# Kernel tuning notes

Measured on AMD Instinct MI355X. Metric: run time of the kernel, lower is better.

Reference implementation:

```python
import jax, jax.numpy as jnp
import numpy as np

B, C, H, W = 32, 512, 32, 32
N_WORDS, WORD_DIM = 77, 256
HW2 = H * W


def setup_inputs() -> dict:
    key = jax.random.key(0)
    k1, k2, k3 = jax.random.split(key, 3)
    feat = jax.random.normal(k1, (B, C, H, W), dtype=jnp.float32)
    word_emb = jax.random.normal(k2, (B, N_WORDS, WORD_DIM), dtype=jnp.float32)
    # nn.Linear(word_dim, img_hw*img_hw): weight (out,in), bias (out,)
    W_fc = jax.random.normal(k3, (HW2, WORD_DIM), dtype=jnp.float32) * (1.0 / np.sqrt(WORD_DIM))
    b_fc = jnp.zeros((HW2,), dtype=jnp.float32)
    return {"feat": feat, "word_emb": word_emb, "W_fc": W_fc, "b_fc": b_fc}


def reference(feat, word_emb, W_fc, b_fc):
    b, c, h, w = feat.shape
    f = feat.reshape(b, c, h * w)                                   # (b, c, hw2)
    we = jnp.einsum('bnd,kd->bnk', word_emb, W_fc) + b_fc           # (b, n, hw2)
    we = jnp.swapaxes(we, 1, 2)                                     # (b, hw2, n)
    scores = jnp.einsum('bck,bkn->bcn', f, we)                      # (b, c, n)
    att = jax.nn.softmax(scores, axis=-1)                           # (b, c, n)
    att_feat = jnp.einsum('bcn,bkn->bck', att, we)                  # (b, c, hw2)
    return att_feat.reshape(b, c, h, w)
```

## Files before the change

kernel.cpp:

```cpp
#include <hip/hip_runtime.h>

#define B_    32
#define C_    512
#define HW2_  1024
#define NW    77
#define NP    80
#define NPT   96
#define WD    256

typedef unsigned int   uint32;
typedef unsigned short u16;
typedef __attribute__((ext_vector_type(8))) short bf16x8;
typedef __attribute__((ext_vector_type(4))) float f32x4;

#define MFMA(a, b, c) __builtin_amdgcn_mfma_f32_16x16x32_bf16(a, b, c, 0, 0, 0)

#define WE_ELN   ((size_t)B_ * 16 * NP * 8)
#define WET_ELN  ((size_t)B_ * HW2_ * 12)

__device__ __forceinline__ void split1(float x, u16 &h, u16 &l) {
    uint32 u = __float_as_uint(x);
    h = (u16)(u >> 16);
    float r = x - __uint_as_float(u & 0xffff0000u);
    uint32 v = __float_as_uint(r);
    l = (u16)((v + 0x7fffu + ((v >> 16) & 1u)) >> 16);
}

__device__ __forceinline__ void split8(float4 a, float4 b, bf16x8 &h, bf16x8 &l) {
    float v[8] = {a.x, a.y, a.z, a.w, b.x, b.y, b.z, b.w};
    #pragma unroll
    for (int i = 0; i < 8; ++i) {
        u16 hh, ll; split1(v[i], hh, ll);
        h[i] = (short)hh; l[i] = (short)ll;
    }
}

__global__ __launch_bounds__(256, 2) void we_gemm(
    const float* __restrict__ word_emb, const float* __restrict__ W_fc,
    const float* __restrict__ b_fc,
    bf16x8* __restrict__ we_hi, bf16x8* __restrict__ we_lo,
    bf16x8* __restrict__ weT_hi, bf16x8* __restrict__ weT_lo)
{
    __shared__ __align__(16) uint32 HL[NP][68];

    const int id = blockIdx.x;
    const int b  = (id & 7) + 8 * (id >> 7);
    const int q  = (id >> 3) & 15;
    const int kb = q * 64;
    const int t  = threadIdx.x;
    const int w  = t >> 6, lane = t & 63, lr = lane & 15, lg = lane >> 4;
    const int kout = kb + 16 * w + lr;

    const float* wrow = W_fc + kout * WD;
    float4 wx[8], wy[8];
    #pragma unroll
    for (int ks = 0; ks < 8; ++ks) {
        const int dk = ks * 32 + 8 * lg;
        wx[ks] = *(const float4*)(wrow + dk);
        wy[ks] = *(const float4*)(wrow + dk + 4);
    }
    __builtin_amdgcn_sched_barrier(0);

    bf16x8 bh[8], bl[8];
    #pragma unroll
    for (int ks = 0; ks < 8; ++ks) split8(wx[ks], wy[ks], bh[ks], bl[ks]);

    f32x4 acc[5];
    #pragma unroll
    for (int m = 0; m < 5; ++m) acc[m] = (f32x4)0.0f;

    const float* emb = word_emb + b * NW * WD;

    #pragma unroll
    for (int ks = 0; ks < 8; ++ks) {
        const int dk = ks * 32 + 8 * lg;
        bf16x8 ah[5], al[5];
        #pragma unroll
        for (int m = 0; m < 5; ++m) {
            const int n = 16 * m + lr;
            float4 x = make_float4(0.f, 0.f, 0.f, 0.f), y = x;
            if (n < NW) {
                const float* p = emb + n * WD + dk;
                x = *(const float4*)p; y = *(const float4*)(p + 4);
            }
            split8(x, y, ah[m], al[m]);
        }
        #pragma unroll
        for (int m = 0; m < 5; ++m) {
            acc[m] = MFMA(ah[m], bh[ks], acc[m]);
            acc[m] = MFMA(ah[m], bl[ks], acc[m]);
            acc[m] = MFMA(al[m], bh[ks], acc[m]);
            acc[m] = MFMA(al[m], bl[ks], acc[m]);
        }
    }

    const float bias = b_fc[kout];
    #pragma unroll
    for (int m = 0; m < 5; ++m)
        #pragma unroll
        for (int r = 0; r < 4; ++r) {
            u16 hh, ll; split1(acc[m][r] + bias, hh, ll);
            HL[16 * m + 4 * lg + r][16 * w + lr] = ((uint32)hh << 16) | ll;
        }
    __syncthreads();

    #pragma unroll
    for (int u0 = 0; u0 < 640; u0 += 256) {
        const int u = u0 + t;
        if (u < 640) {
            const int n = u >> 3, c8 = (u & 7) * 8;
            uint4 p0 = *(const uint4*)&HL[n][c8];
            uint4 p1 = *(const uint4*)&HL[n][c8 + 4];
            const uint32 pw[8] = {p0.x, p0.y, p0.z, p0.w, p1.x, p1.y, p1.z, p1.w};
            bf16x8 hv, lv;
            #pragma unroll
            for (int i = 0; i < 8; ++i) {
                hv[i] = (short)(pw[i] >> 16);
                lv[i] = (short)(pw[i] & 0xffffu);
            }
            const int o = ((b * 16 + q) * NP + n) * 8 + (u & 7);
            we_hi[o] = hv; we_lo[o] = lv;
        }
    }
    #pragma unroll
    for (int v0 = 0; v0 < 1536; v0 += 256) {
        const int v = v0 + t;
        const int sel = v >= 768;
        const int r2  = sel ? v - 768 : v;
        const int row = r2 / 12, g = r2 % 12;
        bf16x8 val;
        #pragma unroll
        for (int i = 0; i < 8; ++i) {
            const int n = g * 8 + i;
            const uint32 p = (n < NP) ? HL[n][row] : 0u;
            val[i] = (short)(sel ? (p & 0xffffu) : (p >> 16));
        }
        (sel ? weT_lo : weT_hi)[(b * HW2_ + kb + row) * 12 + g] = val;
    }
}

__global__ __launch_bounds__(256, 2) void attn_mfma(
    const float* __restrict__ feat,
    const bf16x8* __restrict__ we_hi, const bf16x8* __restrict__ we_lo,
    const bf16x8* __restrict__ weT_hi, const bf16x8* __restrict__ weT_lo,
    float* __restrict__ out)
{
    __shared__ __align__(16) float S[4][16][84];
    __shared__ __align__(16) u16   Ph[32][NPT];
    __shared__ __align__(16) u16   Pl[32][NPT];

    const int id  = blockIdx.x;
    const int b   = (id & 7) + 8 * (id >> 7);
    const int c0  = ((id >> 3) & 15) * 32;

    const int t    = threadIdx.x;
    const int h    = t >> 6;
    const int lane = t & 63, lr = lane & 15, lg = lane >> 4;

    const float* frow0 = feat + (size_t)(b * C_ + c0 + lr) * HW2_;
    const float* frow1 = frow0 + 16 * HW2_;

    float4 f0x[8], f0y[8], f1x[8], f1y[8];
    #pragma unroll
    for (int ks = 0; ks < 8; ++ks) {
        const int kk = h * 256 + ks * 32 + 8 * lg;
        f0x[ks] = *(const float4*)(frow0 + kk);
        f0y[ks] = *(const float4*)(frow0 + kk + 4);
        f1x[ks] = *(const float4*)(frow1 + kk);
        f1y[ks] = *(const float4*)(frow1 + kk + 4);
    }
    __builtin_amdgcn_sched_barrier(0);

    f32x4 acc[2][5];
    #pragma unroll
    for (int s = 0; s < 2; ++s)
        #pragma unroll
        for (int m = 0; m < 5; ++m) acc[s][m] = (f32x4)0.0f;

    #pragma unroll
    for (int ks = 0; ks < 8; ++ks) {
        bf16x8 fh0, fl0, fh1, fl1;
        split8(f0x[ks], f0y[ks], fh0, fl0);
        split8(f1x[ks], f1y[ks], fh1, fl1);
        const int qb  = (b * 16 + h * 4 + (ks >> 1)) * NP;
        const int sub = (ks & 1) * 4 + lg;
        #pragma unroll
        for (int m = 0; m < 5; ++m) {
            const int o = (qb + 16 * m + lr) * 8 + sub;
            const bf16x8 ah = we_hi[o];
            const bf16x8 al = we_lo[o];
            acc[0][m] = MFMA(ah, fh0, acc[0][m]);
            acc[0][m] = MFMA(ah, fl0, acc[0][m]);
            acc[0][m] = MFMA(al, fh0, acc[0][m]);
            acc[1][m] = MFMA(ah, fh1, acc[1][m]);
            acc[1][m] = MFMA(ah, fl1, acc[1][m]);
            acc[1][m] = MFMA(al, fh1, acc[1][m]);
        }
    }

    #pragma unroll
    for (int s = 0; s < 2; ++s) {
        #pragma unroll
        for (int m = 0; m < 5; ++m)
            #pragma unroll
            for (int r = 0; r < 4; ++r)
                S[h][lr][16 * m + 4 * lg + r] = acc[s][m][r];
        __syncthreads();
        {
            const int srow = 4 * h + (lane >> 4), scol = lane & 15;
            float v5[6];
            float mx = -3.0e38f;
            #pragma unroll
            for (int j = 0; j < 6; ++j) {
                const int n = scol + 16 * j;
                float sv = 0.f;
                if (j < 5) {
                    sv = S[0][srow][n] + S[1][srow][n] + S[2][srow][n] + S[3][srow][n];
                    if (n < NW) mx = fmaxf(mx, sv);
                }
                v5[j] = sv;
            }
            mx = fmaxf(mx, __shfl_xor(mx, 1));
            mx = fmaxf(mx, __shfl_xor(mx, 2));
            mx = fmaxf(mx, __shfl_xor(mx, 4));
            mx = fmaxf(mx, __shfl_xor(mx, 8));
            float sum = 0.f;
            #pragma unroll
            for (int j = 0; j < 6; ++j) {
                const int n = scol + 16 * j;
                const float e = (n < NW) ? __expf(v5[j] - mx) : 0.f;
                v5[j] = e; sum += e;
            }
            sum += __shfl_xor(sum, 1);
            sum += __shfl_xor(sum, 2);
            sum += __shfl_xor(sum, 4);
            sum += __shfl_xor(sum, 8);
            const float inv = 1.0f / sum;
            #pragma unroll
            for (int j = 0; j < 6; ++j) {
                const int n = scol + 16 * j;
                u16 ph, pl; split1(v5[j] * inv, ph, pl);
                Ph[16 * s + srow][n] = ph; Pl[16 * s + srow][n] = pl;
            }
        }
        __syncthreads();
    }

    bf16x8 pbh[2][3], pbl[2][3];
    #pragma unroll
    for (int s = 0; s < 2; ++s)
        #pragma unroll
        for (int ksn = 0; ksn < 3; ++ksn) {
            pbh[s][ksn] = *(const bf16x8*)&Ph[16 * s + lr][32 * ksn + 8 * lg];
            pbl[s][ksn] = *(const bf16x8*)&Pl[16 * s + lr][32 * ksn + 8 * lg];
        }
    const bf16x8* th = weT_hi + (size_t)b * HW2_ * 12;
    const bf16x8* tl = weT_lo + (size_t)b * HW2_ * 12;
    float* orow0 = out + (size_t)(b * C_ + c0 + lr) * HW2_;
    float* orow1 = orow0 + 16 * HW2_;

    #pragma unroll
    for (int tt = 0; tt < 16; ++tt) {
        const int row = h * 256 + tt * 16 + lr;
        bf16x8 wa[3], wb[3];
        #pragma unroll
        for (int ksn = 0; ksn < 3; ++ksn) {
            wa[ksn] = th[row * 12 + 4 * ksn + lg];
            wb[ksn] = tl[row * 12 + 4 * ksn + lg];
        }
        f32x4 o0 = (f32x4)0.0f, o1 = (f32x4)0.0f;
        #pragma unroll
        for (int ksn = 0; ksn < 3; ++ksn) {
            o0 = MFMA(wa[ksn], pbh[0][ksn], o0);
            o0 = MFMA(wa[ksn], pbl[0][ksn], o0);
            o0 = MFMA(wb[ksn], pbh[0][ksn], o0);
            o1 = MFMA(wa[ksn], pbh[1][ksn], o1);
            o1 = MFMA(wa[ksn], pbl[1][ksn], o1);
            o1 = MFMA(wb[ksn], pbh[1][ksn], o1);
        }
        const int col = h * 256 + tt * 16 + 4 * lg;
        *(float4*)(orow0 + col) = make_float4(o0[0], o0[1], o0[2], o0[3]);
        *(float4*)(orow1 + col) = make_float4(o1[0], o1[1], o1[2], o1[3]);
    }
}

extern "C" void kernel_launch(void* const* d_in, const int* in_sizes, int n_in,
                              void* d_out, int out_size, void* d_ws, size_t ws_size,
                              hipStream_t stream) {
    (void)in_sizes; (void)n_in; (void)out_size; (void)ws_size;
    const float* feat     = (const float*)d_in[0];
    const float* word_emb = (const float*)d_in[1];
    const float* W_fc     = (const float*)d_in[2];
    const float* b_fc     = (const float*)d_in[3];

    bf16x8* we_hi  = (bf16x8*)d_ws;
    bf16x8* we_lo  = we_hi  + WE_ELN;
    bf16x8* weT_hi = we_lo  + WE_ELN;
    bf16x8* weT_lo = weT_hi + WET_ELN;

    we_gemm<<<512, 256, 0, stream>>>(word_emb, W_fc, b_fc, we_hi, we_lo, weT_hi, weT_lo);
    attn_mfma<<<512, 256, 0, stream>>>(feat, we_hi, we_lo, weT_hi, weT_lo, (float*)d_out);
}
```

Before: 184.3 us.

## Software-pipeline global loads with register ring buffers and scheduling barriers

Restructures the inner loops of both kernels into prefetch pipelines. The word-embedding GEMM double-buffers embedding loads. The attention kernel now streams feature loads three stages deep instead of preloading all of them, and double-buffers the we tiles. The output stage triple-buffers the weT loads. Scheduling barriers pin the load and MFMA order so that memory latency overlaps with the matrix ops. The kernels hold fewer feature registers up front but keep more loads in flight, and the barriers can block useful reordering by the compiler.

```diff
diff --git a/kernel.cpp b/kernel.cpp
--- a/kernel.cpp
+++ b/kernel.cpp
@@ -14,6 +14,7 @@
 typedef __attribute__((ext_vector_type(4))) float f32x4;
 
 #define MFMA(a, b, c) __builtin_amdgcn_mfma_f32_16x16x32_bf16(a, b, c, 0, 0, 0)
+#define SWALL() __builtin_amdgcn_sched_barrier(0)
 
 #define WE_ELN   ((size_t)B_ * 16 * NP * 8)
 #define WET_ELN  ((size_t)B_ * HW2_ * 12)
@@ -59,8 +60,7 @@
         wx[ks] = *(const float4*)(wrow + dk);
         wy[ks] = *(const float4*)(wrow + dk + 4);
     }
-    __builtin_amdgcn_sched_barrier(0);
-
+    SWALL();
     bf16x8 bh[8], bl[8];
     #pragma unroll
     for (int ks = 0; ks < 8; ++ks) split8(wx[ks], wy[ks], bh[ks], bl[ks]);
@@ -71,20 +71,32 @@
 
     const float* emb = word_emb + b * NW * WD;
 
+    float4 ex[2][5], ey[2][5];
+#define WG_E(sl, ksv) do {                                          \
+        const int dk_ = (ksv) * 32 + 8 * lg;                        \
+        _Pragma("unroll")                                           \
+        for (int m_ = 0; m_ < 5; ++m_) {                            \
+            const int n_ = 16 * m_ + lr;                            \
+            if (n_ < NW) {                                          \
+                const float* p_ = emb + n_ * WD + dk_;              \
+                ex[sl][m_] = *(const float4*)p_;                    \
+                ey[sl][m_] = *(const float4*)(p_ + 4);              \
+            } else {                                                \
+                ex[sl][m_] = make_float4(0.f, 0.f, 0.f, 0.f);       \
+                ey[sl][m_] = make_float4(0.f, 0.f, 0.f, 0.f);       \
+            }                                                       \
+        } } while (0)
+
+    WG_E(0, 0);
+    SWALL();
     #pragma unroll
     for (int ks = 0; ks < 8; ++ks) {
-        const int dk = ks * 32 + 8 * lg;
+        const int cur = ks & 1;
+        if (ks < 7) WG_E(cur ^ 1, ks + 1);
+        SWALL();
         bf16x8 ah[5], al[5];
         #pragma unroll
-        for (int m = 0; m < 5; ++m) {
-            const int n = 16 * m + lr;
-            float4 x = make_float4(0.f, 0.f, 0.f, 0.f), y = x;
-            if (n < NW) {
-                const float* p = emb + n * WD + dk;
-                x = *(const float4*)p; y = *(const float4*)(p + 4);
-            }
-            split8(x, y, ah[m], al[m]);
-        }
+        for (int m = 0; m < 5; ++m) split8(ex[cur][m], ey[cur][m], ah[m], al[m]);
         #pragma unroll
         for (int m = 0; m < 5; ++m) {
             acc[m] = MFMA(ah[m], bh[ks], acc[m]);
@@ -92,7 +104,9 @@
             acc[m] = MFMA(al[m], bh[ks], acc[m]);
             acc[m] = MFMA(al[m], bl[ks], acc[m]);
         }
-    }
+        SWALL();
+    }
+#undef WG_E
 
     const float bias = b_fc[kout];
     #pragma unroll
@@ -160,43 +174,55 @@
     const float* frow0 = feat + (size_t)(b * C_ + c0 + lr) * HW2_;
     const float* frow1 = frow0 + 16 * HW2_;
 
-    float4 f0x[8], f0y[8], f1x[8], f1y[8];
+    float4 fx0[3], fy0[3], fx1[3], fy1[3];
+    bf16x8 wph[2][5], wpl[2][5];
+
+#define P1_FEAT(sl, ksv) do {                                       \
+        const int kk_ = h * 256 + (ksv) * 32 + 8 * lg;              \
+        fx0[sl] = *(const float4*)(frow0 + kk_);                    \
+        fy0[sl] = *(const float4*)(frow0 + kk_ + 4);                \
+        fx1[sl] = *(const float4*)(frow1 + kk_);                    \
+        fy1[sl] = *(const float4*)(frow1 + kk_ + 4); } while (0)
+#define P1_WE(sl, ksv) do {                                         \
+        const int qb_  = (b * 16 + h * 4 + ((ksv) >> 1)) * NP;      \
+        const int sub_ = ((ksv) & 1) * 4 + lg;                      \
+        _Pragma("unroll")                                           \
+        for (int m_ = 0; m_ < 5; ++m_) {                            \
+            const int o_ = (qb_ + 16 * m_ + lr) * 8 + sub_;         \
+            wph[sl][m_] = we_hi[o_];                                \
+            wpl[sl][m_] = we_lo[o_];                                \
+        } } while (0)
+
+    f32x4 acc[2][5];
+    #pragma unroll
+    for (int s = 0; s < 2; ++s)
+        #pragma unroll
+        for (int m = 0; m < 5; ++m) acc[s][m] = (f32x4)0.0f;
+
+    P1_FEAT(0, 0); P1_FEAT(1, 1); P1_WE(0, 0);
+    SWALL();
     #pragma unroll
     for (int ks = 0; ks < 8; ++ks) {
-        const int kk = h * 256 + ks * 32 + 8 * lg;
-        f0x[ks] = *(const float4*)(frow0 + kk);
-        f0y[ks] = *(const float4*)(frow0 + kk + 4);
-        f1x[ks] = *(const float4*)(frow1 + kk);
-        f1y[ks] = *(const float4*)(frow1 + kk + 4);
-    }
-    __builtin_amdgcn_sched_barrier(0);
-
-    f32x4 acc[2][5];
-    #pragma unroll
-    for (int s = 0; s < 2; ++s)
-        #pragma unroll
-        for (int m = 0; m < 5; ++m) acc[s][m] = (f32x4)0.0f;
-
-    #pragma unroll
-    for (int ks = 0; ks < 8; ++ks) {
+        const int fc = ks % 3, wc = ks & 1;
+        if (ks < 6) P1_FEAT((ks + 2) % 3, ks + 2);
+        if (ks < 7) P1_WE(wc ^ 1, ks + 1);
+        SWALL();
         bf16x8 fh0, fl0, fh1, fl1;
-        split8(f0x[ks], f0y[ks], fh0, fl0);
-        split8(f1x[ks], f1y[ks], fh1, fl1);
-        const int qb  = (b * 16 + h * 4 + (ks >> 1)) * NP;
-        const int sub = (ks & 1) * 4 + lg;
+        split8(fx0[fc], fy0[fc], fh0, fl0);
+        split8(fx1[fc], fy1[fc], fh1, fl1);
         #pragma unroll
         for (int m = 0; m < 5; ++m) {
-            const int o = (qb + 16 * m + lr) * 8 + sub;
-            const bf16x8 ah = we_hi[o];
-            const bf16x8 al = we_lo[o];
-            acc[0][m] = MFMA(ah, fh0, acc[0][m]);
-            acc[0][m] = MFMA(ah, fl0, acc[0][m]);
-            acc[0][m] = MFMA(al, fh0, acc[0][m]);
-            acc[1][m] = MFMA(ah, fh1, acc[1][m]);
-            acc[1][m] = MFMA(ah, fl1, acc[1][m]);
-            acc[1][m] = MFMA(al, fh1, acc[1][m]);
-        }
-    }
+            acc[0][m] = MFMA(wph[wc][m], fh0, acc[0][m]);
+            acc[0][m] = MFMA(wph[wc][m], fl0, acc[0][m]);
+            acc[0][m] = MFMA(wpl[wc][m], fh0, acc[0][m]);
+            acc[1][m] = MFMA(wph[wc][m], fh1, acc[1][m]);
+            acc[1][m] = MFMA(wph[wc][m], fl1, acc[1][m]);
+            acc[1][m] = MFMA(wpl[wc][m], fh1, acc[1][m]);
+        }
+        SWALL();
+    }
+#undef P1_FEAT
+#undef P1_WE
 
     #pragma unroll
     for (int s = 0; s < 2; ++s) {
@@ -259,29 +285,38 @@
     float* orow0 = out + (size_t)(b * C_ + c0 + lr) * HW2_;
     float* orow1 = orow0 + 16 * HW2_;
 
+    bf16x8 wa[3][3], wb[3][3];
+#define P3_LOAD(sl, ttv) do {                                       \
+        const int row_ = h * 256 + (ttv) * 16 + lr;                 \
+        _Pragma("unroll")                                           \
+        for (int k_ = 0; k_ < 3; ++k_) {                            \
+            wa[sl][k_] = th[row_ * 12 + 4 * k_ + lg];               \
+            wb[sl][k_] = tl[row_ * 12 + 4 * k_ + lg];               \
+        } } while (0)
+
+    P3_LOAD(0, 0); P3_LOAD(1, 1);
+    SWALL();
     #pragma unroll
     for (int tt = 0; tt < 16; ++tt) {
-        const int row = h * 256 + tt * 16 + lr;
-        bf16x8 wa[3], wb[3];
+        const int cur = tt % 3;
+        if (tt < 14) P3_LOAD((tt + 2) % 3, tt + 2);
+        SWALL();
+        f32x4 o0 = (f32x4)0.0f, o1 = (f32x4)0.0f;
         #pragma unroll
         for (int ksn = 0; ksn < 3; ++ksn) {
-            wa[ksn] = th[row * 12 + 4 * ksn + lg];
-            wb[ksn] = tl[row * 12 + 4 * ksn + lg];
-        }
-        f32x4 o0 = (f32x4)0.0f, o1 = (f32x4)0.0f;
-        #pragma unroll
-        for (int ksn = 0; ksn < 3; ++ksn) {
-            o0 = MFMA(wa[ksn], pbh[0][ksn], o0);
-            o0 = MFMA(wa[ksn], pbl[0][ksn], o0);
-            o0 = MFMA(wb[ksn], pbh[0][ksn], o0);
-            o1 = MFMA(wa[ksn], pbh[1][ksn], o1);
-            o1 = MFMA(wa[ksn], pbl[1][ksn], o1);
-            o1 = MFMA(wb[ksn], pbh[1][ksn], o1);
+            o0 = MFMA(wa[cur][ksn], pbh[0][ksn], o0);
+            o0 = MFMA(wa[cur][ksn], pbl[0][ksn], o0);
+            o0 = MFMA(wb[cur][ksn], pbh[0][ksn], o0);
+            o1 = MFMA(wa[cur][ksn], pbh[1][ksn], o1);
+            o1 = MFMA(wa[cur][ksn], pbl[1][ksn], o1);
+            o1 = MFMA(wb[cur][ksn], pbh[1][ksn], o1);
         }
         const int col = h * 256 + tt * 16 + 4 * lg;
         *(float4*)(orow0 + col) = make_float4(o0[0], o0[1], o0[2], o0[3]);
         *(float4*)(orow1 + col) = make_float4(o1[0], o1[1], o1[2], o1[3]);
-    }
+        SWALL();
+    }
+#undef P3_LOAD
 }
 
 extern "C" void kernel_launch(void* const* d_in, const int* in_sizes, int n_in,
```

New measurement: 179.8 us. -2.5%, faster.

## Double threads per block to 512 and split work across eight waves

Applied to the files above, without the earlier changes.

Both kernels move from 256 to 512 threads per block. In the weight-embedding GEMM, the word-row tiles are split between two wave halves. In the attention kernel, the feature K-dimension and the output columns are split across eight waves, and the softmax reduces eight partial score tiles. The upfront feature prefetch is replaced with per-step loads to reduce register pressure. The aim is more waves in flight to hide memory latency, at the cost of a larger shared-memory reduction and less load batching.

```diff
diff --git a/kernel.cpp b/kernel.cpp
--- a/kernel.cpp
+++ b/kernel.cpp
@@ -14,6 +14,7 @@
 typedef __attribute__((ext_vector_type(4))) float f32x4;
 
 #define MFMA(a, b, c) __builtin_amdgcn_mfma_f32_16x16x32_bf16(a, b, c, 0, 0, 0)
+#define SWALL() __builtin_amdgcn_sched_barrier(0)
 
 #define WE_ELN   ((size_t)B_ * 16 * NP * 8)
 #define WET_ELN  ((size_t)B_ * HW2_ * 12)
@@ -35,7 +36,7 @@
     }
 }
 
-__global__ __launch_bounds__(256, 2) void we_gemm(
+__global__ __launch_bounds__(512, 4) void we_gemm(
     const float* __restrict__ word_emb, const float* __restrict__ W_fc,
     const float* __restrict__ b_fc,
     bf16x8* __restrict__ we_hi, bf16x8* __restrict__ we_lo,
@@ -48,82 +49,91 @@
     const int q  = (id >> 3) & 15;
     const int kb = q * 64;
     const int t  = threadIdx.x;
-    const int w  = t >> 6, lane = t & 63, lr = lane & 15, lg = lane >> 4;
+    const int h  = t >> 6;
+    const int w  = h & 3, nh = h >> 2;
+    const int lane = t & 63, lr = lane & 15, lg = lane >> 4;
     const int kout = kb + 16 * w + lr;
+    const int m0 = nh ? 3 : 0;
+    const int mc = nh ? 2 : 3;
 
     const float* wrow = W_fc + kout * WD;
-    float4 wx[8], wy[8];
+    bf16x8 bh[8], bl[8];
+    #pragma unroll
+    for (int c = 0; c < 2; ++c) {
+        float4 wx[4], wy[4];
+        #pragma unroll
+        for (int i = 0; i < 4; ++i) {
+            const int dk = (c * 4 + i) * 32 + 8 * lg;
+            wx[i] = *(const float4*)(wrow + dk);
+            wy[i] = *(const float4*)(wrow + dk + 4);
+        }
+        SWALL();
+        #pragma unroll
+        for (int i = 0; i < 4; ++i) split8(wx[i], wy[i], bh[c * 4 + i], bl[c * 4 + i]);
+    }
+
+    f32x4 acc[3];
+    #pragma unroll
+    for (int mm = 0; mm < 3; ++mm) acc[mm] = (f32x4)0.0f;
+
+    const float* emb = word_emb + b * NW * WD;
+
     #pragma unroll
     for (int ks = 0; ks < 8; ++ks) {
         const int dk = ks * 32 + 8 * lg;
-        wx[ks] = *(const float4*)(wrow + dk);
-        wy[ks] = *(const float4*)(wrow + dk + 4);
-    }
-    __builtin_amdgcn_sched_barrier(0);
-
-    bf16x8 bh[8], bl[8];
-    #pragma unroll
-    for (int ks = 0; ks < 8; ++ks) split8(wx[ks], wy[ks], bh[ks], bl[ks]);
-
-    f32x4 acc[5];
-    #pragma unroll
-    for (int m = 0; m < 5; ++m) acc[m] = (f32x4)0.0f;
-
-    const float* emb = word_emb + b * NW * WD;
-
-    #pragma unroll
-    for (int ks = 0; ks < 8; ++ks) {
-        const int dk = ks * 32 + 8 * lg;
-        bf16x8 ah[5], al[5];
-        #pragma unroll
-        for (int m = 0; m < 5; ++m) {
-            const int n = 16 * m + lr;
-            float4 x = make_float4(0.f, 0.f, 0.f, 0.f), y = x;
-            if (n < NW) {
-                const float* p = emb + n * WD + dk;
-                x = *(const float4*)p; y = *(const float4*)(p + 4);
-            }
-            split8(x, y, ah[m], al[m]);
-        }
-        #pragma unroll
-        for (int m = 0; m < 5; ++m) {
-            acc[m] = MFMA(ah[m], bh[ks], acc[m]);
-            acc[m] = MFMA(ah[m], bl[ks], acc[m]);
-            acc[m] = MFMA(al[m], bh[ks], acc[m]);
-            acc[m] = MFMA(al[m], bl[ks], acc[m]);
+        bf16x8 ah[3], al[3];
+        #pragma unroll
+        for (int mm = 0; mm < 3; ++mm) {
+            if (mm < mc) {
+                const int n = 16 * (m0 + mm) + lr;
+                float4 x = make_float4(0.f, 0.f, 0.f, 0.f), y = x;
+                if (n < NW) {
+                    const float* p = emb + n * WD + dk;
+                    x = *(const float4*)p; y = *(const float4*)(p + 4);
+                }
+                split8(x, y, ah[mm], al[mm]);
+            }
+        }
+        #pragma unroll
+        for (int mm = 0; mm < 3; ++mm) {
+            if (mm < mc) {
+                acc[mm] = MFMA(ah[mm], bh[ks], acc[mm]);
+                acc[mm] = MFMA(ah[mm], bl[ks], acc[mm]);
+                acc[mm] = MFMA(al[mm], bh[ks], acc[mm]);
+                acc[mm] = MFMA(al[mm], bl[ks], acc[mm]);
+            }
         }
     }
 
     const float bias = b_fc[kout];
     #pragma unroll
-    for (int m = 0; m < 5; ++m)
-        #pragma unroll
-        for (int r = 0; r < 4; ++r) {
-            u16 hh, ll; split1(acc[m][r] + bias, hh, ll);
-            HL[16 * m + 4 * lg + r][16 * w + lr] = ((uint32)hh << 16) | ll;
-        }
+    for (int mm = 0; mm < 3; ++mm) {
+        if (mm < mc) {
+            #pragma unroll
+            for (int r = 0; r < 4; ++r) {
+                u16 hh, ll; split1(acc[mm][r] + bias, hh, ll);
+                HL[16 * (m0 + mm) + 4 * lg + r][16 * w + lr] = ((uint32)hh << 16) | ll;
+            }
+        }
+    }
     __syncthreads();
 
-    #pragma unroll
-    for (int u0 = 0; u0 < 640; u0 += 256) {
-        const int u = u0 + t;
-        if (u < 640) {
-            const int n = u >> 3, c8 = (u & 7) * 8;
-            uint4 p0 = *(const uint4*)&HL[n][c8];
-            uint4 p1 = *(const uint4*)&HL[n][c8 + 4];
-            const uint32 pw[8] = {p0.x, p0.y, p0.z, p0.w, p1.x, p1.y, p1.z, p1.w};
-            bf16x8 hv, lv;
-            #pragma unroll
-            for (int i = 0; i < 8; ++i) {
-                hv[i] = (short)(pw[i] >> 16);
-                lv[i] = (short)(pw[i] & 0xffffu);
-            }
-            const int o = ((b * 16 + q) * NP + n) * 8 + (u & 7);
-            we_hi[o] = hv; we_lo[o] = lv;
-        }
-    }
-    #pragma unroll
-    for (int v0 = 0; v0 < 1536; v0 += 256) {
+    for (int u = t; u < 640; u += 512) {
+        const int n = u >> 3, c8 = (u & 7) * 8;
+        uint4 p0 = *(const uint4*)&HL[n][c8];
+        uint4 p1 = *(const uint4*)&HL[n][c8 + 4];
+        const uint32 pw[8] = {p0.x, p0.y, p0.z, p0.w, p1.x, p1.y, p1.z, p1.w};
+        bf16x8 hv, lv;
+        #pragma unroll
+        for (int i = 0; i < 8; ++i) {
+            hv[i] = (short)(pw[i] >> 16);
+            lv[i] = (short)(pw[i] & 0xffffu);
+        }
+        const int o = ((b * 16 + q) * NP + n) * 8 + (u & 7);
+        we_hi[o] = hv; we_lo[o] = lv;
+    }
+    #pragma unroll
+    for (int v0 = 0; v0 < 1536; v0 += 512) {
         const int v = v0 + t;
         const int sel = v >= 768;
         const int r2  = sel ? v - 768 : v;
@@ -139,13 +149,13 @@
     }
 }
 
-__global__ __launch_bounds__(256, 2) void attn_mfma(
+__global__ __launch_bounds__(512, 4) void attn_mfma(
     const float* __restrict__ feat,
     const bf16x8* __restrict__ we_hi, const bf16x8* __restrict__ we_lo,
     const bf16x8* __restrict__ weT_hi, const bf16x8* __restrict__ weT_lo,
     float* __restrict__ out)
 {
-    __shared__ __align__(16) float S[4][16][84];
+    __shared__ __align__(16) float S[8][16][84];
     __shared__ __align__(16) u16   Ph[32][NPT];
     __shared__ __align__(16) u16   Pl[32][NPT];
 
@@ -160,17 +170,6 @@
     const float* frow0 = feat + (size_t)(b * C_ + c0 + lr) * HW2_;
     const float* frow1 = frow0 + 16 * HW2_;
 
-    float4 f0x[8], f0y[8], f1x[8], f1y[8];
-    #pragma unroll
-    for (int ks = 0; ks < 8; ++ks) {
-        const int kk = h * 256 + ks * 32 + 8 * lg;
-        f0x[ks] = *(const float4*)(frow0 + kk);
-        f0y[ks] = *(const float4*)(frow0 + kk + 4);
-        f1x[ks] = *(const float4*)(frow1 + kk);
-        f1y[ks] = *(const float4*)(frow1 + kk + 4);
-    }
-    __builtin_amdgcn_sched_barrier(0);
-
     f32x4 acc[2][5];
     #pragma unroll
     for (int s = 0; s < 2; ++s)
@@ -178,11 +177,16 @@
         for (int m = 0; m < 5; ++m) acc[s][m] = (f32x4)0.0f;
 
     #pragma unroll
-    for (int ks = 0; ks < 8; ++ks) {
+    for (int ks = 0; ks < 4; ++ks) {
+        const int kk = h * 128 + ks * 32 + 8 * lg;
         bf16x8 fh0, fl0, fh1, fl1;
-        split8(f0x[ks], f0y[ks], fh0, fl0);
-        split8(f1x[ks], f1y[ks], fh1, fl1);
-        const int qb  = (b * 16 + h * 4 + (ks >> 1)) * NP;
+        {   float4 x = *(const float4*)(frow0 + kk);
+            float4 y = *(const float4*)(frow0 + kk + 4);
+            split8(x, y, fh0, fl0); }
+        {   float4 x = *(const float4*)(frow1 + kk);
+            float4 y = *(const float4*)(frow1 + kk + 4);
+            split8(x, y, fh1, fl1); }
+        const int qb  = (b * 16 + 2 * h + (ks >> 1)) * NP;
         const int sub = (ks & 1) * 4 + lg;
         #pragma unroll
         for (int m = 0; m < 5; ++m) {
@@ -207,39 +211,39 @@
                 S[h][lr][16 * m + 4 * lg + r] = acc[s][m][r];
         __syncthreads();
         {
-            const int srow = 4 * h + (lane >> 4), scol = lane & 15;
-            float v5[6];
+            const int srow = 2 * h + (lane >> 5), col0 = lane & 31;
+            float v3[3];
             float mx = -3.0e38f;
             #pragma unroll
-            for (int j = 0; j < 6; ++j) {
-                const int n = scol + 16 * j;
-                float sv = 0.f;
-                if (j < 5) {
-                    sv = S[0][srow][n] + S[1][srow][n] + S[2][srow][n] + S[3][srow][n];
-                    if (n < NW) mx = fmaxf(mx, sv);
-                }
-                v5[j] = sv;
+            for (int j = 0; j < 3; ++j) {
+                const int n = col0 + 32 * j;
+                float sv = S[0][srow][n] + S[1][srow][n] + S[2][srow][n] + S[3][srow][n]
+                         + S[4][srow][n] + S[5][srow][n] + S[6][srow][n] + S[7][srow][n];
+                if (n < NW) mx = fmaxf(mx, sv);
+                v3[j] = sv;
             }
             mx = fmaxf(mx, __shfl_xor(mx, 1));
             mx = fmaxf(mx, __shfl_xor(mx, 2));
             mx = fmaxf(mx, __shfl_xor(mx, 4));
             mx = fmaxf(mx, __shfl_xor(mx, 8));
+            mx = fmaxf(mx, __shfl_xor(mx, 16));
             float sum = 0.f;
             #pragma unroll
-            for (int j = 0; j < 6; ++j) {
-                const int n = scol + 16 * j;
-                const float e = (n < NW) ? __expf(v5[j] - mx) : 0.f;
-                v5[j] = e; sum += e;
+            for (int j = 0; j < 3; ++j) {
+                const int n = col0 + 32 * j;
+                const float e = (n < NW) ? __expf(v3[j] - mx) : 0.f;
+                v3[j] = e; sum += e;
             }
             sum += __shfl_xor(sum, 1);
             sum += __shfl_xor(sum, 2);
             sum += __shfl_xor(sum, 4);
             sum += __shfl_xor(sum, 8);
+            sum += __shfl_xor(sum, 16);
             const float inv = 1.0f / sum;
             #pragma unroll
-            for (int j = 0; j < 6; ++j) {
-                const int n = scol + 16 * j;
-                u16 ph, pl; split1(v5[j] * inv, ph, pl);
+            for (int j = 0; j < 3; ++j) {
+                const int n = col0 + 32 * j;
+                u16 ph, pl; split1(v3[j] * inv, ph, pl);
                 Ph[16 * s + srow][n] = ph; Pl[16 * s + srow][n] = pl;
             }
         }
@@ -260,8 +264,8 @@
     float* orow1 = orow0 + 16 * HW2_;
 
     #pragma unroll
-    for (int tt = 0; tt < 16; ++tt) {
-        const int row = h * 256 + tt * 16 + lr;
+    for (int tt = 0; tt < 8; ++tt) {
+        const int row = h * 128 + tt * 16 + lr;
         bf16x8 wa[3], wb[3];
         #pragma unroll
         for (int ksn = 0; ksn < 3; ++ksn) {
@@ -278,7 +282,7 @@
             o1 = MFMA(wa[ksn], pbl[1][ksn], o1);
             o1 = MFMA(wb[ksn], pbh[1][ksn], o1);
         }
-        const int col = h * 256 + tt * 16 + 4 * lg;
+        const int col = h * 128 + tt * 16 + 4 * lg;
         *(float4*)(orow0 + col) = make_float4(o0[0], o0[1], o0[2], o0[3]);
         *(float4*)(orow1 + col) = make_float4(o1[0], o1[1], o1[2], o1[3]);
     }
@@ -298,6 +302,6 @@
     bf16x8* weT_hi = we_lo  + WE_ELN;
     bf16x8* weT_lo = weT_hi + WET_ELN;
 
-    we_gemm<<<512, 256, 0, stream>>>(word_emb, W_fc, b_fc, we_hi, we_lo, weT_hi, weT_lo);
-    attn_mfma<<<512, 256, 0, stream>>>(feat, we_hi, we_lo, weT_hi, weT_lo, (float*)d_out);
-}
+    we_gemm<<<512, 512, 0, stream>>>(word_emb, W_fc, b_fc, we_hi, we_lo, weT_hi, weT_lo);
+    attn_mfma<<<512, 512, 0, stream>>>(feat, we_hi, we_lo, weT_hi, weT_lo, (float*)d_out);
+}
```

Measured after the change: 179.4 us. 1.03x faster.
